# Performance work log

Hardware: AMD Instinct MI355X
Metric: run time of the kernel (lower is better)

## Reference

```python
import jax, jax.numpy as jnp
import numpy as np

B, T, H, DH = 4, 2048, 16, 128
D = H * DH            # inner_dim = 2048
F = 4096              # mlp_inner_dim
E = 8                 # num_expert_mlp
TOP_K = 2


def setup_inputs() -> dict:
    key = jax.random.key(0)
    ks = jax.random.split(key, 5)
    s_in = 1.0 / np.sqrt(D)
    s_f = 1.0 / np.sqrt(F)
    return {
        "stm": jax.random.normal(ks[0], (B, T, H, DH), dtype=jnp.float32),
        "gate_w": jax.random.normal(ks[1], (E, D), dtype=jnp.float32) * s_in,
        "w1": jax.random.normal(ks[2], (E, F, D), dtype=jnp.float32) * s_in,
        "w2": jax.random.normal(ks[3], (E, D, F), dtype=jnp.float32) * s_f,
        "w3": jax.random.normal(ks[4], (E, F, D), dtype=jnp.float32) * s_in,
    }


def reference(stm, gate_w, w1, w2, w3):
    b, t, h, dh = stm.shape
    d = h * dh
    x = stm.reshape(b * t, d)                                   # [N, D]
    logits = x @ gate_w.T                                       # [N, E]
    top_logit, top_idx = jax.lax.top_k(logits, TOP_K)           # [N, 2]
    gw = jax.nn.softmax(top_logit.astype(jnp.float32), axis=1).astype(x.dtype)
    out = jnp.zeros_like(x)
    n_expert = w1.shape[0]
    for e in range(n_expert):
        # combine weight for expert e per token (0 if not routed)
        we = jnp.sum(jnp.where(top_idx == e, gw, jnp.zeros_like(gw)), axis=1)  # [N]
        gate = jax.nn.silu(x @ w1[e].T)                          # [N, F]
        up = x @ w3[e].T                                         # [N, F]
        y = (gate * up) @ w2[e].T                                # [N, D]
        out = out + we[:, None] * y
    return out.reshape(b, t, h, dh)
```

## Files before the change

kernel.cpp:

```cpp
#include <hip/hip_runtime.h>
#include <hip/hip_bf16.h>
#include <stdint.h>

#define N_TOK 8192
#define DIM   2048
#define FDIM  4096
#define NEXP  8

#define XB_OFF   0ull
#define HB_OFF   33554432ull
#define WB1_OFF  176160768ull
#define WB3_OFF  243269632ull
#define META_OFF 310378496ull
#define CNT_OFF   (META_OFF)
#define EBASE_OFF (META_OFF + 64ull)
#define ELIST_OFF (META_OFF + 128ull)
#define EWTS_OFF  (ELIST_OFF + 262144ull)

typedef float f32x4 __attribute__((ext_vector_type(4)));
typedef short s16x8 __attribute__((ext_vector_type(8)));

__device__ __forceinline__ uint32_t pkbf(float a, float b) {
  uint32_t ua = __builtin_bit_cast(uint32_t, a) + 0x8000u;
  uint32_t ub = __builtin_bit_cast(uint32_t, b) + 0x8000u;
  return (ua >> 16) | (ub & 0xffff0000u);
}

__device__ __forceinline__ void gld16(const void* g, void* l) {
  __builtin_amdgcn_global_load_lds(
      (__attribute__((address_space(1))) void*)g,
      (__attribute__((address_space(3))) void*)l, 16, 0, 0);
}

__global__ void zero_out_k(float* out) {
  const size_t i = ((size_t)blockIdx.x * 256 + threadIdx.x) * 4;
  *(float4*)(out + i) = make_float4(0.f, 0.f, 0.f, 0.f);
}

__global__ void init_k(int* cnt) {
  if (threadIdx.x < NEXP) cnt[threadIdx.x] = 0;
}

__global__ void router_k(const float* __restrict__ x, const float* __restrict__ gw,
                         __hip_bfloat16* __restrict__ xb, int* __restrict__ cnt,
                         int* __restrict__ elist, float* __restrict__ ewts) {
  const int n = blockIdx.x;
  const int t = threadIdx.x;
  const float* xr = x + (size_t)n * DIM;
  const float4 v0 = *(const float4*)(xr + t * 8);
  const float4 v1 = *(const float4*)(xr + t * 8 + 4);
  uint4 u;
  u.x = pkbf(v0.x, v0.y); u.y = pkbf(v0.z, v0.w);
  u.z = pkbf(v1.x, v1.y); u.w = pkbf(v1.z, v1.w);
  *(uint4*)(xb + (size_t)n * DIM + t * 8) = u;

  float p[NEXP];
#pragma unroll
  for (int e = 0; e < NEXP; ++e) {
    const float* g = gw + e * DIM + t * 8;
    const float4 g0 = *(const float4*)g;
    const float4 g1 = *(const float4*)(g + 4);
    p[e] = v0.x * g0.x + v0.y * g0.y + v0.z * g0.z + v0.w * g0.w +
           v1.x * g1.x + v1.y * g1.y + v1.z * g1.z + v1.w * g1.w;
  }
#pragma unroll
  for (int off = 32; off >= 1; off >>= 1)
#pragma unroll
    for (int e = 0; e < NEXP; ++e) p[e] += __shfl_xor(p[e], off, 64);

  __shared__ float red[4][NEXP];
  const int lane = t & 63, wv = t >> 6;
  if (lane == 0) {
#pragma unroll
    for (int e = 0; e < NEXP; ++e) red[wv][e] = p[e];
  }
  __syncthreads();
  if (t == 0) {
    float l0 = -1e30f, l1 = -1e30f;
    int e0 = 0, e1 = 0;
#pragma unroll
    for (int e = 0; e < NEXP; ++e) {
      float v = red[0][e] + red[1][e] + red[2][e] + red[3][e];
      if (v > l0) { l1 = l0; e1 = e0; l0 = v; e0 = e; }
      else if (v > l1) { l1 = v; e1 = e; }
    }
    const float ed = expf(l1 - l0);
    const float inv = 1.f / (1.f + ed);
    int s0 = atomicAdd(cnt + e0, 1);
    elist[e0 * N_TOK + s0] = n;
    ewts[e0 * N_TOK + s0] = inv;
    int s1 = atomicAdd(cnt + e1, 1);
    elist[e1 * N_TOK + s1] = (int)((uint32_t)n | 0x80000000u);
    ewts[e1 * N_TOK + s1] = ed * inv;
  }
}

__global__ void scan_k(const int* __restrict__ cnt, int* __restrict__ ebase) {
  if (threadIdx.x == 0 && blockIdx.x == 0) {
    int b = 0;
    for (int e = 0; e < NEXP; ++e) { ebase[e] = b; b += (cnt[e] + 127) & ~127; }
  }
}

__global__ void convW_k(const float* __restrict__ src, __hip_bfloat16* __restrict__ dst,
                        int r0, int nrh, int rtot, int kd) {
  const int cpr = kd / 8;
  const int total = NEXP * nrh * cpr;
  for (int i = blockIdx.x * blockDim.x + threadIdx.x; i < total;
       i += gridDim.x * blockDim.x) {
    const int e = i / (nrh * cpr);
    const int rem = i - e * nrh * cpr;
    const int lr = rem / cpr;
    const int c = rem - lr * cpr;
    const float* s = src + ((size_t)e * rtot + r0 + lr) * (size_t)kd + c * 8;
    const float4 a = *(const float4*)s;
    const float4 b = *(const float4*)(s + 4);
    uint4 u;
    u.x = pkbf(a.x, a.y); u.y = pkbf(a.z, a.w);
    u.z = pkbf(b.x, b.y); u.w = pkbf(b.z, b.w);
    *(uint4*)(dst + ((size_t)e * nrh + lr) * (size_t)kd + c * 8) = u;
  }
}

__global__ __launch_bounds__(256, 2) void moe_up_k(
    const __hip_bfloat16* __restrict__ xb, const __hip_bfloat16* __restrict__ w1b,
    const __hip_bfloat16* __restrict__ w3b, __hip_bfloat16* __restrict__ hb,
    const int* __restrict__ cnt, const int* __restrict__ ebase,
    const int* __restrict__ elist, int noff) {
  constexpr int NT = DIM / 32;
  const int e = blockIdx.z;
  const int count = cnt[e];
  const int mt = blockIdx.y;
  if (mt * 128 >= count) return;
  const int bn0 = blockIdx.x * 128;
  const int ncol0 = noff + bn0;

  __shared__ char lds[73728];
  const int t = threadIdx.x;
  const int lane = t & 63, wv = t >> 6;
  const int wr = wv >> 1, wc = wv & 1;
  const int* lst = elist + e * N_TOK;
  const size_t hrow0 = (size_t)ebase[e] + (size_t)mt * 128;

  const int r0 = t >> 2;
  const int ks = (t & 3) ^ ((r0 >> 1) & 3);
  size_t sA[2], sB1[2];
  int ldsO[2];
#pragma unroll
  for (int i = 0; i < 2; ++i) {
    const int r = r0 + i * 64;
    int idx = mt * 128 + r;
    if (idx >= count) idx = 0;
    const size_t tok = (size_t)(lst[idx] & 0x7fffffff);
    sA[i] = tok * DIM + ks * 8;
    sB1[i] = ((size_t)e * 2048 + bn0 + r) * DIM + ks * 8;
    ldsO[i] = i * 4096 + wv * 1024;
  }

  const int fr = lane & 15;
  const int swzc = ((lane >> 4) ^ ((fr >> 1) & 3)) << 4;
  const int aoff = (wr * 64 + fr) * 64 + swzc;
  const int boff = (wc * 64 + fr) * 64 + swzc;

  f32x4 accG[4][4], accU[4][4];
#pragma unroll
  for (int mi = 0; mi < 4; ++mi)
#pragma unroll
    for (int ni = 0; ni < 4; ++ni) {
      accG[mi][ni] = {0.f, 0.f, 0.f, 0.f};
      accU[mi][ni] = {0.f, 0.f, 0.f, 0.f};
    }

  auto stage = [&](int kt, int b) {
    const int k0 = kt * 32;
    char* base = lds + b * 24576;
#pragma unroll
    for (int i = 0; i < 2; ++i)
      gld16(xb + sA[i] + k0, base + ldsO[i]);
#pragma unroll
    for (int i = 0; i < 2; ++i)
      gld16(w1b + sB1[i] + k0, base + 8192 + ldsO[i]);
#pragma unroll
    for (int i = 0; i < 2; ++i)
      gld16(w3b + sB1[i] + k0, base + 16384 + ldsO[i]);
  };

  stage(0, 0);
  stage(1, 1);
  asm volatile("s_waitcnt vmcnt(6)" ::: "memory");
  __builtin_amdgcn_sched_barrier(0);
  __builtin_amdgcn_s_barrier();
  __builtin_amdgcn_sched_barrier(0);

  int bR = 0, bS = 2;
#pragma unroll 3
  for (int kt = 0; kt < NT; ++kt) {
    const int t2 = (kt + 2 < NT) ? kt + 2 : NT - 1;
    stage(t2, bS);
    char* base = lds + bR * 24576;
    s16x8 af[4], b1f[4], b3f[4];
#pragma unroll
    for (int mi = 0; mi < 4; ++mi)
      af[mi] = *(const s16x8*)(base + aoff + mi * 1024);
#pragma unroll
    for (int ni = 0; ni < 4; ++ni) {
      b1f[ni] = *(const s16x8*)(base + 8192 + boff + ni * 1024);
      b3f[ni] = *(const s16x8*)(base + 16384 + boff + ni * 1024);
    }
#pragma unroll
    for (int mi = 0; mi < 4; ++mi)
#pragma unroll
      for (int ni = 0; ni < 4; ++ni) {
        accG[mi][ni] = __builtin_amdgcn_mfma_f32_16x16x32_bf16(
            af[mi], b1f[ni], accG[mi][ni], 0, 0, 0);
        accU[mi][ni] = __builtin_amdgcn_mfma_f32_16x16x32_bf16(
            af[mi], b3f[ni], accU[mi][ni], 0, 0, 0);
      }
    asm volatile("s_waitcnt vmcnt(6)" ::: "memory");
    __builtin_amdgcn_sched_barrier(0);
    __builtin_amdgcn_s_barrier();
    __builtin_amdgcn_sched_barrier(0);
    bR = (bR == 2) ? 0 : bR + 1;
    bS = (bS == 2) ? 0 : bS + 1;
  }

  const int erow = (lane >> 4) * 4;
  const int ecol = lane & 15;
#pragma unroll
  for (int mi = 0; mi < 4; ++mi)
#pragma unroll
    for (int ni = 0; ni < 4; ++ni) {
      const size_t cb = ncol0 + wc * 64 + ni * 16 + ecol;
#pragma unroll
      for (int j = 0; j < 4; ++j) {
        const size_t r = hrow0 + wr * 64 + mi * 16 + erow + j;
        const float g = accG[mi][ni][j];
        const float uu = accU[mi][ni][j];
        const float h = g / (1.f + __expf(-g)) * uu;
        hb[r * FDIM + cb] = __float2bfloat16(h);
      }
    }
}

__global__ __launch_bounds__(256, 2) void moe_down_k(
    const __hip_bfloat16* __restrict__ hb, const __hip_bfloat16* __restrict__ w2b,
    float* __restrict__ out, const int* __restrict__ cnt,
    const int* __restrict__ ebase, const int* __restrict__ elist,
    const float* __restrict__ ewts) {
  constexpr int NT = FDIM / 32;
  const int e = blockIdx.x;
  const int count = cnt[e];
  const int mt = blockIdx.y;
  if (mt * 128 >= count) return;
  const int bn0 = blockIdx.z * 256;

  __shared__ char lds[73728];
  const int t = threadIdx.x;
  const int lane = t & 63, wv = t >> 6;
  const int wr = wv >> 1, wc = wv & 1;
  const int* lst = elist + e * N_TOK;
  const size_t hrow0 = (size_t)ebase[e] + (size_t)mt * 128;

  const int r0 = t >> 2;
  const int ks = (t & 3) ^ ((r0 >> 1) & 3);
  size_t sA[2], sB[2];
  int ldsO[2];
#pragma unroll
  for (int i = 0; i < 2; ++i) {
    const int r = r0 + i * 64;
    sA[i] = (hrow0 + r) * (size_t)FDIM + ks * 8;
    sB[i] = ((size_t)e * 2048 + bn0 + r) * (size_t)FDIM + ks * 8;
    ldsO[i] = i * 4096 + wv * 1024;
  }
  const size_t sBp = 128 * (size_t)FDIM;

  const int fr = lane & 15;
  const int swzc = ((lane >> 4) ^ ((fr >> 1) & 3)) << 4;
  const int aoff = (wr * 64 + fr) * 64 + swzc;
  const int boff = (wc * 64 + fr) * 64 + swzc;

  f32x4 accP[2][4][4];
#pragma unroll
  for (int p = 0; p < 2; ++p)
#pragma unroll
    for (int mi = 0; mi < 4; ++mi)
#pragma unroll
      for (int ni = 0; ni < 4; ++ni) accP[p][mi][ni] = {0.f, 0.f, 0.f, 0.f};

  auto stage = [&](int kt, int b) {
    const int k0 = kt * 32;
    char* base = lds + b * 24576;
#pragma unroll
    for (int i = 0; i < 2; ++i)
      gld16(hb + sA[i] + k0, base + ldsO[i]);
#pragma unroll
    for (int i = 0; i < 2; ++i)
      gld16(w2b + sB[i] + k0, base + 8192 + ldsO[i]);
#pragma unroll
    for (int i = 0; i < 2; ++i)
      gld16(w2b + sB[i] + sBp + k0, base + 16384 + ldsO[i]);
  };

  stage(0, 0);
  stage(1, 1);
  asm volatile("s_waitcnt vmcnt(6)" ::: "memory");
  __builtin_amdgcn_sched_barrier(0);
  __builtin_amdgcn_s_barrier();
  __builtin_amdgcn_sched_barrier(0);

  int bR = 0, bS = 2;
#pragma unroll 3
  for (int kt = 0; kt < NT; ++kt) {
    const int t2 = (kt + 2 < NT) ? kt + 2 : NT - 1;
    stage(t2, bS);
    char* base = lds + bR * 24576;
    s16x8 af[4], b0f[4], b1f[4];
#pragma unroll
    for (int mi = 0; mi < 4; ++mi)
      af[mi] = *(const s16x8*)(base + aoff + mi * 1024);
#pragma unroll
    for (int ni = 0; ni < 4; ++ni) {
      b0f[ni] = *(const s16x8*)(base + 8192 + boff + ni * 1024);
      b1f[ni] = *(const s16x8*)(base + 16384 + boff + ni * 1024);
    }
#pragma unroll
    for (int mi = 0; mi < 4; ++mi)
#pragma unroll
      for (int ni = 0; ni < 4; ++ni) {
        accP[0][mi][ni] = __builtin_amdgcn_mfma_f32_16x16x32_bf16(
            af[mi], b0f[ni], accP[0][mi][ni], 0, 0, 0);
        accP[1][mi][ni] = __builtin_amdgcn_mfma_f32_16x16x32_bf16(
            af[mi], b1f[ni], accP[1][mi][ni], 0, 0, 0);
      }
    asm volatile("s_waitcnt vmcnt(6)" ::: "memory");
    __builtin_amdgcn_sched_barrier(0);
    __builtin_amdgcn_s_barrier();
    __builtin_amdgcn_sched_barrier(0);
    bR = (bR == 2) ? 0 : bR + 1;
    bS = (bS == 2) ? 0 : bS + 1;
  }

  const int erow = (lane >> 4) * 4;
  const int ecol = lane & 15;
#pragma unroll
  for (int mi = 0; mi < 4; ++mi)
#pragma unroll
    for (int j = 0; j < 4; ++j) {
      const int i = mt * 128 + wr * 64 + mi * 16 + erow + j;
      if (i < count) {
        const uint32_t info = (uint32_t)lst[i];
        const int tok = (int)(info & 0x7fffffffu);
        const float wt = ewts[e * N_TOK + i];
        float* prow = out + (size_t)tok * DIM;
#pragma unroll
        for (int p = 0; p < 2; ++p)
#pragma unroll
          for (int ni = 0; ni < 4; ++ni) {
            const int cb = bn0 + p * 128 + wc * 64 + ni * 16 + ecol;
            atomicAdd(prow + cb, wt * accP[p][mi][ni][j]);
          }
      }
    }
}

extern "C" void kernel_launch(void* const* d_in, const int* in_sizes, int n_in,
                              void* d_out, int out_size, void* d_ws, size_t ws_size,
                              hipStream_t stream) {
  const float* stm = (const float*)d_in[0];
  const float* gw = (const float*)d_in[1];
  const float* w1 = (const float*)d_in[2];
  const float* w2 = (const float*)d_in[3];
  const float* w3 = (const float*)d_in[4];
  float* out = (float*)d_out;
  char* ws = (char*)d_ws;

  __hip_bfloat16* xb = (__hip_bfloat16*)(ws + XB_OFF);
  __hip_bfloat16* hb = (__hip_bfloat16*)(ws + HB_OFF);
  __hip_bfloat16* wb1 = (__hip_bfloat16*)(ws + WB1_OFF);
  __hip_bfloat16* wb3 = (__hip_bfloat16*)(ws + WB3_OFF);
  __hip_bfloat16* w2full = (__hip_bfloat16*)(ws + WB1_OFF);
  int* cnt = (int*)(ws + CNT_OFF);
  int* ebase = (int*)(ws + EBASE_OFF);
  int* elist = (int*)(ws + ELIST_OFF);
  float* ewts = (float*)(ws + EWTS_OFF);

  init_k<<<1, 64, 0, stream>>>(cnt);
  router_k<<<N_TOK, 256, 0, stream>>>(stm, gw, xb, cnt, elist, ewts);
  scan_k<<<1, 64, 0, stream>>>(cnt, ebase);
  zero_out_k<<<N_TOK * DIM / 1024, 256, 0, stream>>>(out);

  const dim3 gUp(16, 64, 8);
  const dim3 gDn(8, 64, 8);

  convW_k<<<2048, 256, 0, stream>>>(w1, wb1, 0, 2048, FDIM, DIM);
  convW_k<<<2048, 256, 0, stream>>>(w3, wb3, 0, 2048, FDIM, DIM);
  moe_up_k<<<gUp, 256, 0, stream>>>(xb, wb1, wb3, hb, cnt, ebase, elist, 0);
  convW_k<<<2048, 256, 0, stream>>>(w1, wb1, 2048, 2048, FDIM, DIM);
  convW_k<<<2048, 256, 0, stream>>>(w3, wb3, 2048, 2048, FDIM, DIM);
  moe_up_k<<<gUp, 256, 0, stream>>>(xb, wb1, wb3, hb, cnt, ebase, elist, 2048);

  convW_k<<<4096, 256, 0, stream>>>(w2, w2full, 0, 2048, DIM, FDIM);
  moe_down_k<<<gDn, 256, 0, stream>>>(hb, w2full, out, cnt, ebase, elist, ewts);
}
```

Before: 1.349 ms.

## Overlap fp32-to-bf16 weight conversion with GEMM kernels via double-buffered quarters

Removes the standalone weight-conversion and zeroing kernels. The conversion of the next weight quarter (or half) now runs inside extra blocks of the preceding router, up-projection or down-projection launch, using two ping-pong workspace buffers. Output zeroing is folded into the router launch as well. The aim is to hide conversion bandwidth behind GEMM compute and cut serial kernel launches. The cost is smaller GEMM launches (four up and two down) with more tail effects, and converter blocks competing with GEMM blocks for the same CUs.

```diff
diff --git a/kernel.cpp b/kernel.cpp
--- a/kernel.cpp
+++ b/kernel.cpp
@@ -9,14 +9,16 @@
 
 #define XB_OFF   0ull
 #define HB_OFF   33554432ull
-#define WB1_OFF  176160768ull
-#define WB3_OFF  243269632ull
+#define WQ0_OFF  176160768ull
+#define WQ1_OFF  243269632ull
 #define META_OFF 310378496ull
 #define CNT_OFF   (META_OFF)
 #define EBASE_OFF (META_OFF + 64ull)
 #define ELIST_OFF (META_OFF + 128ull)
 #define EWTS_OFF  (ELIST_OFF + 262144ull)
 
+#define W3Q_ELEMS 16777216
+
 typedef float f32x4 __attribute__((ext_vector_type(4)));
 typedef short s16x8 __attribute__((ext_vector_type(8)));
 
@@ -32,82 +34,11 @@
       (__attribute__((address_space(3))) void*)l, 16, 0, 0);
 }
 
-__global__ void zero_out_k(float* out) {
-  const size_t i = ((size_t)blockIdx.x * 256 + threadIdx.x) * 4;
-  *(float4*)(out + i) = make_float4(0.f, 0.f, 0.f, 0.f);
-}
-
-__global__ void init_k(int* cnt) {
-  if (threadIdx.x < NEXP) cnt[threadIdx.x] = 0;
-}
-
-__global__ void router_k(const float* __restrict__ x, const float* __restrict__ gw,
-                         __hip_bfloat16* __restrict__ xb, int* __restrict__ cnt,
-                         int* __restrict__ elist, float* __restrict__ ewts) {
-  const int n = blockIdx.x;
-  const int t = threadIdx.x;
-  const float* xr = x + (size_t)n * DIM;
-  const float4 v0 = *(const float4*)(xr + t * 8);
-  const float4 v1 = *(const float4*)(xr + t * 8 + 4);
-  uint4 u;
-  u.x = pkbf(v0.x, v0.y); u.y = pkbf(v0.z, v0.w);
-  u.z = pkbf(v1.x, v1.y); u.w = pkbf(v1.z, v1.w);
-  *(uint4*)(xb + (size_t)n * DIM + t * 8) = u;
-
-  float p[NEXP];
-#pragma unroll
-  for (int e = 0; e < NEXP; ++e) {
-    const float* g = gw + e * DIM + t * 8;
-    const float4 g0 = *(const float4*)g;
-    const float4 g1 = *(const float4*)(g + 4);
-    p[e] = v0.x * g0.x + v0.y * g0.y + v0.z * g0.z + v0.w * g0.w +
-           v1.x * g1.x + v1.y * g1.y + v1.z * g1.z + v1.w * g1.w;
-  }
-#pragma unroll
-  for (int off = 32; off >= 1; off >>= 1)
-#pragma unroll
-    for (int e = 0; e < NEXP; ++e) p[e] += __shfl_xor(p[e], off, 64);
-
-  __shared__ float red[4][NEXP];
-  const int lane = t & 63, wv = t >> 6;
-  if (lane == 0) {
-#pragma unroll
-    for (int e = 0; e < NEXP; ++e) red[wv][e] = p[e];
-  }
-  __syncthreads();
-  if (t == 0) {
-    float l0 = -1e30f, l1 = -1e30f;
-    int e0 = 0, e1 = 0;
-#pragma unroll
-    for (int e = 0; e < NEXP; ++e) {
-      float v = red[0][e] + red[1][e] + red[2][e] + red[3][e];
-      if (v > l0) { l1 = l0; e1 = e0; l0 = v; e0 = e; }
-      else if (v > l1) { l1 = v; e1 = e; }
-    }
-    const float ed = expf(l1 - l0);
-    const float inv = 1.f / (1.f + ed);
-    int s0 = atomicAdd(cnt + e0, 1);
-    elist[e0 * N_TOK + s0] = n;
-    ewts[e0 * N_TOK + s0] = inv;
-    int s1 = atomicAdd(cnt + e1, 1);
-    elist[e1 * N_TOK + s1] = (int)((uint32_t)n | 0x80000000u);
-    ewts[e1 * N_TOK + s1] = ed * inv;
-  }
-}
-
-__global__ void scan_k(const int* __restrict__ cnt, int* __restrict__ ebase) {
-  if (threadIdx.x == 0 && blockIdx.x == 0) {
-    int b = 0;
-    for (int e = 0; e < NEXP; ++e) { ebase[e] = b; b += (cnt[e] + 127) & ~127; }
-  }
-}
-
-__global__ void convW_k(const float* __restrict__ src, __hip_bfloat16* __restrict__ dst,
-                        int r0, int nrh, int rtot, int kd) {
+__device__ __forceinline__ void conv_chunks(
+    const float* __restrict__ src, __hip_bfloat16* __restrict__ dst,
+    int r0, int nrh, int rtot, int kd, int idx0, int stride, int total) {
   const int cpr = kd / 8;
-  const int total = NEXP * nrh * cpr;
-  for (int i = blockIdx.x * blockDim.x + threadIdx.x; i < total;
-       i += gridDim.x * blockDim.x) {
+  for (int i = idx0; i < total; i += stride) {
     const int e = i / (nrh * cpr);
     const int rem = i - e * nrh * cpr;
     const int lr = rem / cpr;
@@ -122,18 +53,112 @@
   }
 }
 
+__global__ void init_k(int* cnt) {
+  if (threadIdx.x < NEXP) cnt[threadIdx.x] = 0;
+}
+
+__global__ void router_k(const float* __restrict__ x, const float* __restrict__ gw,
+                         __hip_bfloat16* __restrict__ xb, int* __restrict__ cnt,
+                         int* __restrict__ elist, float* __restrict__ ewts,
+                         const float* __restrict__ w1, const float* __restrict__ w3,
+                         __hip_bfloat16* __restrict__ wq0, float* __restrict__ out) {
+  const int blk = blockIdx.x;
+  const int t = threadIdx.x;
+  if (blk >= N_TOK) {
+    const int cb = blk - N_TOK;
+    if (cb < 2048) {
+      conv_chunks(w1, wq0, 0, 1024, FDIM, DIM, cb * 256 + t, 2048 * 256, 2097152);
+    } else if (cb < 4096) {
+      conv_chunks(w3, wq0 + W3Q_ELEMS, 0, 1024, FDIM, DIM,
+                  (cb - 2048) * 256 + t, 2048 * 256, 2097152);
+    } else {
+      for (size_t i = (size_t)(cb - 4096) * 256 + t; i < 4194304; i += 512 * 256)
+        *(float4*)(out + i * 4) = make_float4(0.f, 0.f, 0.f, 0.f);
+    }
+    return;
+  }
+  const int n = blk;
+  const float* xr = x + (size_t)n * DIM;
+  const float4 v0 = *(const float4*)(xr + t * 8);
+  const float4 v1 = *(const float4*)(xr + t * 8 + 4);
+  uint4 u;
+  u.x = pkbf(v0.x, v0.y); u.y = pkbf(v0.z, v0.w);
+  u.z = pkbf(v1.x, v1.y); u.w = pkbf(v1.z, v1.w);
+  *(uint4*)(xb + (size_t)n * DIM + t * 8) = u;
+
+  float p[NEXP];
+#pragma unroll
+  for (int e = 0; e < NEXP; ++e) {
+    const float* g = gw + e * DIM + t * 8;
+    const float4 g0 = *(const float4*)g;
+    const float4 g1 = *(const float4*)(g + 4);
+    p[e] = v0.x * g0.x + v0.y * g0.y + v0.z * g0.z + v0.w * g0.w +
+           v1.x * g1.x + v1.y * g1.y + v1.z * g1.z + v1.w * g1.w;
+  }
+#pragma unroll
+  for (int off = 32; off >= 1; off >>= 1)
+#pragma unroll
+    for (int e = 0; e < NEXP; ++e) p[e] += __shfl_xor(p[e], off, 64);
+
+  __shared__ float red[4][NEXP];
+  const int lane = t & 63, wv = t >> 6;
+  if (lane == 0) {
+#pragma unroll
+    for (int e = 0; e < NEXP; ++e) red[wv][e] = p[e];
+  }
+  __syncthreads();
+  if (t == 0) {
+    float l0 = -1e30f, l1 = -1e30f;
+    int e0 = 0, e1 = 0;
+#pragma unroll
+    for (int e = 0; e < NEXP; ++e) {
+      float v = red[0][e] + red[1][e] + red[2][e] + red[3][e];
+      if (v > l0) { l1 = l0; e1 = e0; l0 = v; e0 = e; }
+      else if (v > l1) { l1 = v; e1 = e; }
+    }
+    const float ed = expf(l1 - l0);
+    const float inv = 1.f / (1.f + ed);
+    int s0 = atomicAdd(cnt + e0, 1);
+    elist[e0 * N_TOK + s0] = n;
+    ewts[e0 * N_TOK + s0] = inv;
+    int s1 = atomicAdd(cnt + e1, 1);
+    elist[e1 * N_TOK + s1] = (int)((uint32_t)n | 0x80000000u);
+    ewts[e1 * N_TOK + s1] = ed * inv;
+  }
+}
+
+__global__ void scan_k(const int* __restrict__ cnt, int* __restrict__ ebase) {
+  if (threadIdx.x == 0 && blockIdx.x == 0) {
+    int b = 0;
+    for (int e = 0; e < NEXP; ++e) { ebase[e] = b; b += (cnt[e] + 127) & ~127; }
+  }
+}
+
 __global__ __launch_bounds__(256, 2) void moe_up_k(
-    const __hip_bfloat16* __restrict__ xb, const __hip_bfloat16* __restrict__ w1b,
-    const __hip_bfloat16* __restrict__ w3b, __hip_bfloat16* __restrict__ hb,
-    const int* __restrict__ cnt, const int* __restrict__ ebase,
-    const int* __restrict__ elist, int noff) {
+    const __hip_bfloat16* __restrict__ xb, const __hip_bfloat16* __restrict__ wq,
+    __hip_bfloat16* __restrict__ wnext, const float* __restrict__ w1,
+    const float* __restrict__ w3, const float* __restrict__ w2,
+    __hip_bfloat16* __restrict__ hb, const int* __restrict__ cnt,
+    const int* __restrict__ ebase, const int* __restrict__ elist, int qn) {
   constexpr int NT = DIM / 32;
+  if (blockIdx.x >= 8) {
+    const int cb = (blockIdx.x - 8) + 8 * (blockIdx.y + 64 * blockIdx.z);
+    const int idx0 = cb * 256 + threadIdx.x;
+    if (qn < 3) {
+      const int r0 = (qn + 1) * 1024;
+      conv_chunks(w1, wnext, r0, 1024, FDIM, DIM, idx0, 4096 * 256, 2097152);
+      conv_chunks(w3, wnext + W3Q_ELEMS, r0, 1024, FDIM, DIM, idx0, 4096 * 256, 2097152);
+    } else {
+      conv_chunks(w2, wnext, 0, 1024, DIM, FDIM, idx0, 4096 * 256, 4194304);
+    }
+    return;
+  }
   const int e = blockIdx.z;
   const int count = cnt[e];
   const int mt = blockIdx.y;
   if (mt * 128 >= count) return;
   const int bn0 = blockIdx.x * 128;
-  const int ncol0 = noff + bn0;
+  const int ncol0 = qn * 1024 + bn0;
 
   __shared__ char lds[73728];
   const int t = threadIdx.x;
@@ -153,7 +178,7 @@
     if (idx >= count) idx = 0;
     const size_t tok = (size_t)(lst[idx] & 0x7fffffff);
     sA[i] = tok * DIM + ks * 8;
-    sB1[i] = ((size_t)e * 2048 + bn0 + r) * DIM + ks * 8;
+    sB1[i] = ((size_t)e * 1024 + bn0 + r) * DIM + ks * 8;
     ldsO[i] = i * 4096 + wv * 1024;
   }
 
@@ -179,10 +204,10 @@
       gld16(xb + sA[i] + k0, base + ldsO[i]);
 #pragma unroll
     for (int i = 0; i < 2; ++i)
-      gld16(w1b + sB1[i] + k0, base + 8192 + ldsO[i]);
-#pragma unroll
-    for (int i = 0; i < 2; ++i)
-      gld16(w3b + sB1[i] + k0, base + 16384 + ldsO[i]);
+      gld16(wq + sB1[i] + k0, base + 8192 + ldsO[i]);
+#pragma unroll
+    for (int i = 0; i < 2; ++i)
+      gld16(wq + W3Q_ELEMS + sB1[i] + k0, base + 16384 + ldsO[i]);
   };
 
   stage(0, 0);
@@ -243,11 +268,18 @@
 }
 
 __global__ __launch_bounds__(256, 2) void moe_down_k(
-    const __hip_bfloat16* __restrict__ hb, const __hip_bfloat16* __restrict__ w2b,
+    const __hip_bfloat16* __restrict__ hb, const __hip_bfloat16* __restrict__ w2h,
+    __hip_bfloat16* __restrict__ wnext, const float* __restrict__ w2,
     float* __restrict__ out, const int* __restrict__ cnt,
     const int* __restrict__ ebase, const int* __restrict__ elist,
-    const float* __restrict__ ewts) {
+    const float* __restrict__ ewts, int half) {
   constexpr int NT = FDIM / 32;
+  if (blockIdx.z >= 4) {
+    const int cb = blockIdx.x + 8 * (blockIdx.y + 64 * (blockIdx.z - 4));
+    conv_chunks(w2, wnext, 1024, 1024, DIM, FDIM,
+                cb * 256 + threadIdx.x, 2048 * 256, 4194304);
+    return;
+  }
   const int e = blockIdx.x;
   const int count = cnt[e];
   const int mt = blockIdx.y;
@@ -269,7 +301,7 @@
   for (int i = 0; i < 2; ++i) {
     const int r = r0 + i * 64;
     sA[i] = (hrow0 + r) * (size_t)FDIM + ks * 8;
-    sB[i] = ((size_t)e * 2048 + bn0 + r) * (size_t)FDIM + ks * 8;
+    sB[i] = ((size_t)e * 1024 + bn0 + r) * (size_t)FDIM + ks * 8;
     ldsO[i] = i * 4096 + wv * 1024;
   }
   const size_t sBp = 128 * (size_t)FDIM;
@@ -295,10 +327,10 @@
       gld16(hb + sA[i] + k0, base + ldsO[i]);
 #pragma unroll
     for (int i = 0; i < 2; ++i)
-      gld16(w2b + sB[i] + k0, base + 8192 + ldsO[i]);
-#pragma unroll
-    for (int i = 0; i < 2; ++i)
-      gld16(w2b + sB[i] + sBp + k0, base + 16384 + ldsO[i]);
+      gld16(w2h + sB[i] + k0, base + 8192 + ldsO[i]);
+#pragma unroll
+    for (int i = 0; i < 2; ++i)
+      gld16(w2h + sB[i] + sBp + k0, base + 16384 + ldsO[i]);
   };
 
   stage(0, 0);
@@ -356,7 +388,7 @@
         for (int p = 0; p < 2; ++p)
 #pragma unroll
           for (int ni = 0; ni < 4; ++ni) {
-            const int cb = bn0 + p * 128 + wc * 64 + ni * 16 + ecol;
+            const int cb = half * 1024 + bn0 + p * 128 + wc * 64 + ni * 16 + ecol;
             atomicAdd(prow + cb, wt * accP[p][mi][ni][j]);
           }
       }
@@ -376,29 +408,27 @@
 
   __hip_bfloat16* xb = (__hip_bfloat16*)(ws + XB_OFF);
   __hip_bfloat16* hb = (__hip_bfloat16*)(ws + HB_OFF);
-  __hip_bfloat16* wb1 = (__hip_bfloat16*)(ws + WB1_OFF);
-  __hip_bfloat16* wb3 = (__hip_bfloat16*)(ws + WB3_OFF);
-  __hip_bfloat16* w2full = (__hip_bfloat16*)(ws + WB1_OFF);
+  __hip_bfloat16* wq[2] = {(__hip_bfloat16*)(ws + WQ0_OFF),
+                           (__hip_bfloat16*)(ws + WQ1_OFF)};
   int* cnt = (int*)(ws + CNT_OFF);
   int* ebase = (int*)(ws + EBASE_OFF);
   int* elist = (int*)(ws + ELIST_OFF);
   float* ewts = (float*)(ws + EWTS_OFF);
 
   init_k<<<1, 64, 0, stream>>>(cnt);
-  router_k<<<N_TOK, 256, 0, stream>>>(stm, gw, xb, cnt, elist, ewts);
+  router_k<<<N_TOK + 4608, 256, 0, stream>>>(stm, gw, xb, cnt, elist, ewts,
+                                             w1, w3, wq[0], out);
   scan_k<<<1, 64, 0, stream>>>(cnt, ebase);
-  zero_out_k<<<N_TOK * DIM / 1024, 256, 0, stream>>>(out);
 
   const dim3 gUp(16, 64, 8);
-  const dim3 gDn(8, 64, 8);
-
-  convW_k<<<2048, 256, 0, stream>>>(w1, wb1, 0, 2048, FDIM, DIM);
-  convW_k<<<2048, 256, 0, stream>>>(w3, wb3, 0, 2048, FDIM, DIM);
-  moe_up_k<<<gUp, 256, 0, stream>>>(xb, wb1, wb3, hb, cnt, ebase, elist, 0);
-  convW_k<<<2048, 256, 0, stream>>>(w1, wb1, 2048, 2048, FDIM, DIM);
-  convW_k<<<2048, 256, 0, stream>>>(w3, wb3, 2048, 2048, FDIM, DIM);
-  moe_up_k<<<gUp, 256, 0, stream>>>(xb, wb1, wb3, hb, cnt, ebase, elist, 2048);
-
-  convW_k<<<4096, 256, 0, stream>>>(w2, w2full, 0, 2048, DIM, FDIM);
-  moe_down_k<<<gDn, 256, 0, stream>>>(hb, w2full, out, cnt, ebase, elist, ewts);
-}
+  for (int q = 0; q < 4; ++q)
+    moe_up_k<<<gUp, 256, 0, stream>>>(xb, wq[q & 1], wq[(q + 1) & 1],
+                                      w1, w3, w2, hb, cnt, ebase, elist, q);
+
+  const dim3 gDn0(8, 64, 8);
+  const dim3 gDn1(8, 64, 4);
+  moe_down_k<<<gDn0, 256, 0, stream>>>(hb, wq[0], wq[1], w2, out,
+                                       cnt, ebase, elist, ewts, 0);
+  moe_down_k<<<gDn1, 256, 0, stream>>>(hb, wq[1], wq[1], w2, out,
+                                       cnt, ebase, elist, ewts, 1);
+}
```

New measurement: 1.819 ms. 34.8% more time.

## Fuse weight conversion and output zeroing into router, split down-proj by F halves

Applied to the files above, without the earlier changes.

The first-half w1/w3 bf16 conversion and the output zeroing now run as extra blocks of the router kernel, so they overlap with routing instead of running as separate launches. The w1+w3 conversions for the second half are merged into one kernel. The down projection is split into two K-halves over F, each using a half-size converted slice of w2, with the workspace buffers rotated between halves. This removes launches and tail bubbles and keeps the workspace small, at the cost of two partial down-projection passes that both accumulate into the output.

```diff
diff --git a/kernel.cpp b/kernel.cpp
--- a/kernel.cpp
+++ b/kernel.cpp
@@ -9,8 +9,8 @@
 
 #define XB_OFF   0ull
 #define HB_OFF   33554432ull
-#define WB1_OFF  176160768ull
-#define WB3_OFF  243269632ull
+#define WQA_OFF  176160768ull
+#define WQB_OFF  243269632ull
 #define META_OFF 310378496ull
 #define CNT_OFF   (META_OFF)
 #define EBASE_OFF (META_OFF + 64ull)
@@ -32,82 +32,11 @@
       (__attribute__((address_space(3))) void*)l, 16, 0, 0);
 }
 
-__global__ void zero_out_k(float* out) {
-  const size_t i = ((size_t)blockIdx.x * 256 + threadIdx.x) * 4;
-  *(float4*)(out + i) = make_float4(0.f, 0.f, 0.f, 0.f);
-}
-
-__global__ void init_k(int* cnt) {
-  if (threadIdx.x < NEXP) cnt[threadIdx.x] = 0;
-}
-
-__global__ void router_k(const float* __restrict__ x, const float* __restrict__ gw,
-                         __hip_bfloat16* __restrict__ xb, int* __restrict__ cnt,
-                         int* __restrict__ elist, float* __restrict__ ewts) {
-  const int n = blockIdx.x;
-  const int t = threadIdx.x;
-  const float* xr = x + (size_t)n * DIM;
-  const float4 v0 = *(const float4*)(xr + t * 8);
-  const float4 v1 = *(const float4*)(xr + t * 8 + 4);
-  uint4 u;
-  u.x = pkbf(v0.x, v0.y); u.y = pkbf(v0.z, v0.w);
-  u.z = pkbf(v1.x, v1.y); u.w = pkbf(v1.z, v1.w);
-  *(uint4*)(xb + (size_t)n * DIM + t * 8) = u;
-
-  float p[NEXP];
-#pragma unroll
-  for (int e = 0; e < NEXP; ++e) {
-    const float* g = gw + e * DIM + t * 8;
-    const float4 g0 = *(const float4*)g;
-    const float4 g1 = *(const float4*)(g + 4);
-    p[e] = v0.x * g0.x + v0.y * g0.y + v0.z * g0.z + v0.w * g0.w +
-           v1.x * g1.x + v1.y * g1.y + v1.z * g1.z + v1.w * g1.w;
-  }
-#pragma unroll
-  for (int off = 32; off >= 1; off >>= 1)
-#pragma unroll
-    for (int e = 0; e < NEXP; ++e) p[e] += __shfl_xor(p[e], off, 64);
-
-  __shared__ float red[4][NEXP];
-  const int lane = t & 63, wv = t >> 6;
-  if (lane == 0) {
-#pragma unroll
-    for (int e = 0; e < NEXP; ++e) red[wv][e] = p[e];
-  }
-  __syncthreads();
-  if (t == 0) {
-    float l0 = -1e30f, l1 = -1e30f;
-    int e0 = 0, e1 = 0;
-#pragma unroll
-    for (int e = 0; e < NEXP; ++e) {
-      float v = red[0][e] + red[1][e] + red[2][e] + red[3][e];
-      if (v > l0) { l1 = l0; e1 = e0; l0 = v; e0 = e; }
-      else if (v > l1) { l1 = v; e1 = e; }
-    }
-    const float ed = expf(l1 - l0);
-    const float inv = 1.f / (1.f + ed);
-    int s0 = atomicAdd(cnt + e0, 1);
-    elist[e0 * N_TOK + s0] = n;
-    ewts[e0 * N_TOK + s0] = inv;
-    int s1 = atomicAdd(cnt + e1, 1);
-    elist[e1 * N_TOK + s1] = (int)((uint32_t)n | 0x80000000u);
-    ewts[e1 * N_TOK + s1] = ed * inv;
-  }
-}
-
-__global__ void scan_k(const int* __restrict__ cnt, int* __restrict__ ebase) {
-  if (threadIdx.x == 0 && blockIdx.x == 0) {
-    int b = 0;
-    for (int e = 0; e < NEXP; ++e) { ebase[e] = b; b += (cnt[e] + 127) & ~127; }
-  }
-}
-
-__global__ void convW_k(const float* __restrict__ src, __hip_bfloat16* __restrict__ dst,
-                        int r0, int nrh, int rtot, int kd) {
+__device__ __forceinline__ void conv_chunks(
+    const float* __restrict__ src, __hip_bfloat16* __restrict__ dst,
+    int r0, int nrh, int rtot, int kd, int idx0, int stride, int total) {
   const int cpr = kd / 8;
-  const int total = NEXP * nrh * cpr;
-  for (int i = blockIdx.x * blockDim.x + threadIdx.x; i < total;
-       i += gridDim.x * blockDim.x) {
+  for (int i = idx0; i < total; i += stride) {
     const int e = i / (nrh * cpr);
     const int rem = i - e * nrh * cpr;
     const int lr = rem / cpr;
@@ -119,6 +48,114 @@
     u.x = pkbf(a.x, a.y); u.y = pkbf(a.z, a.w);
     u.z = pkbf(b.x, b.y); u.w = pkbf(b.z, b.w);
     *(uint4*)(dst + ((size_t)e * nrh + lr) * (size_t)kd + c * 8) = u;
+  }
+}
+
+__global__ void init_k(int* cnt) {
+  if (threadIdx.x < NEXP) cnt[threadIdx.x] = 0;
+}
+
+__global__ void convH_k(const float* __restrict__ w1, __hip_bfloat16* __restrict__ d1,
+                        const float* __restrict__ w3, __hip_bfloat16* __restrict__ d3,
+                        int r0) {
+  const int idx0 = blockIdx.x * 256 + threadIdx.x;
+  conv_chunks(w1, d1, r0, 2048, FDIM, DIM, idx0, 4096 * 256, 4194304);
+  conv_chunks(w3, d3, r0, 2048, FDIM, DIM, idx0, 4096 * 256, 4194304);
+}
+
+__global__ void convW2_k(const float* __restrict__ w2, __hip_bfloat16* __restrict__ dst,
+                         int col0) {
+  const int total = NEXP * DIM * 256;
+  for (int i = blockIdx.x * blockDim.x + threadIdx.x; i < total;
+       i += gridDim.x * blockDim.x) {
+    const int e = i / (DIM * 256);
+    const int rem = i - e * DIM * 256;
+    const int lr = rem >> 8;
+    const int c = rem & 255;
+    const float* s = w2 + ((size_t)e * DIM + lr) * (size_t)FDIM + col0 + c * 8;
+    const float4 a = *(const float4*)s;
+    const float4 b = *(const float4*)(s + 4);
+    uint4 u;
+    u.x = pkbf(a.x, a.y); u.y = pkbf(a.z, a.w);
+    u.z = pkbf(b.x, b.y); u.w = pkbf(b.z, b.w);
+    *(uint4*)(dst + ((size_t)e * DIM + lr) * 2048 + c * 8) = u;
+  }
+}
+
+__global__ void router_k(const float* __restrict__ x, const float* __restrict__ gw,
+                         __hip_bfloat16* __restrict__ xb, int* __restrict__ cnt,
+                         int* __restrict__ elist, float* __restrict__ ewts,
+                         const float* __restrict__ w1, const float* __restrict__ w3,
+                         __hip_bfloat16* __restrict__ wA, __hip_bfloat16* __restrict__ wB,
+                         float* __restrict__ out) {
+  const int blk = blockIdx.x;
+  const int t = threadIdx.x;
+  if (blk >= N_TOK) {
+    const int cb = blk - N_TOK;
+    if (cb < 4096) {
+      conv_chunks(w1, wA, 0, 2048, FDIM, DIM, cb * 256 + t, 4096 * 256, 4194304);
+    } else if (cb < 8192) {
+      conv_chunks(w3, wB, 0, 2048, FDIM, DIM, (cb - 4096) * 256 + t, 4096 * 256, 4194304);
+    } else {
+      for (size_t i = (size_t)(cb - 8192) * 256 + t; i < 4194304; i += 512 * 256)
+        *(float4*)(out + i * 4) = make_float4(0.f, 0.f, 0.f, 0.f);
+    }
+    return;
+  }
+  const int n = blk;
+  const float* xr = x + (size_t)n * DIM;
+  const float4 v0 = *(const float4*)(xr + t * 8);
+  const float4 v1 = *(const float4*)(xr + t * 8 + 4);
+  uint4 u;
+  u.x = pkbf(v0.x, v0.y); u.y = pkbf(v0.z, v0.w);
+  u.z = pkbf(v1.x, v1.y); u.w = pkbf(v1.z, v1.w);
+  *(uint4*)(xb + (size_t)n * DIM + t * 8) = u;
+
+  float p[NEXP];
+#pragma unroll
+  for (int e = 0; e < NEXP; ++e) {
+    const float* g = gw + e * DIM + t * 8;
+    const float4 g0 = *(const float4*)g;
+    const float4 g1 = *(const float4*)(g + 4);
+    p[e] = v0.x * g0.x + v0.y * g0.y + v0.z * g0.z + v0.w * g0.w +
+           v1.x * g1.x + v1.y * g1.y + v1.z * g1.z + v1.w * g1.w;
+  }
+#pragma unroll
+  for (int off = 32; off >= 1; off >>= 1)
+#pragma unroll
+    for (int e = 0; e < NEXP; ++e) p[e] += __shfl_xor(p[e], off, 64);
+
+  __shared__ float red[4][NEXP];
+  const int lane = t & 63, wv = t >> 6;
+  if (lane == 0) {
+#pragma unroll
+    for (int e = 0; e < NEXP; ++e) red[wv][e] = p[e];
+  }
+  __syncthreads();
+  if (t == 0) {
+    float l0 = -1e30f, l1 = -1e30f;
+    int e0 = 0, e1 = 0;
+#pragma unroll
+    for (int e = 0; e < NEXP; ++e) {
+      float v = red[0][e] + red[1][e] + red[2][e] + red[3][e];
+      if (v > l0) { l1 = l0; e1 = e0; l0 = v; e0 = e; }
+      else if (v > l1) { l1 = v; e1 = e; }
+    }
+    const float ed = expf(l1 - l0);
+    const float inv = 1.f / (1.f + ed);
+    int s0 = atomicAdd(cnt + e0, 1);
+    elist[e0 * N_TOK + s0] = n;
+    ewts[e0 * N_TOK + s0] = inv;
+    int s1 = atomicAdd(cnt + e1, 1);
+    elist[e1 * N_TOK + s1] = (int)((uint32_t)n | 0x80000000u);
+    ewts[e1 * N_TOK + s1] = ed * inv;
+  }
+}
+
+__global__ void scan_k(const int* __restrict__ cnt, int* __restrict__ ebase) {
+  if (threadIdx.x == 0 && blockIdx.x == 0) {
+    int b = 0;
+    for (int e = 0; e < NEXP; ++e) { ebase[e] = b; b += (cnt[e] + 127) & ~127; }
   }
 }
 
@@ -243,11 +280,11 @@
 }
 
 __global__ __launch_bounds__(256, 2) void moe_down_k(
-    const __hip_bfloat16* __restrict__ hb, const __hip_bfloat16* __restrict__ w2b,
+    const __hip_bfloat16* __restrict__ hb, const __hip_bfloat16* __restrict__ w2h,
     float* __restrict__ out, const int* __restrict__ cnt,
     const int* __restrict__ ebase, const int* __restrict__ elist,
-    const float* __restrict__ ewts) {
-  constexpr int NT = FDIM / 32;
+    const float* __restrict__ ewts, int half) {
+  constexpr int NT = 2048 / 32;
   const int e = blockIdx.x;
   const int count = cnt[e];
   const int mt = blockIdx.y;
@@ -268,11 +305,11 @@
 #pragma unroll
   for (int i = 0; i < 2; ++i) {
     const int r = r0 + i * 64;
-    sA[i] = (hrow0 + r) * (size_t)FDIM + ks * 8;
-    sB[i] = ((size_t)e * 2048 + bn0 + r) * (size_t)FDIM + ks * 8;
+    sA[i] = (hrow0 + r) * (size_t)FDIM + half * 2048 + ks * 8;
+    sB[i] = ((size_t)e * DIM + bn0 + r) * 2048 + ks * 8;
     ldsO[i] = i * 4096 + wv * 1024;
   }
-  const size_t sBp = 128 * (size_t)FDIM;
+  const size_t sBp = 128 * 2048;
 
   const int fr = lane & 15;
   const int swzc = ((lane >> 4) ^ ((fr >> 1) & 3)) << 4;
@@ -295,10 +332,10 @@
       gld16(hb + sA[i] + k0, base + ldsO[i]);
 #pragma unroll
     for (int i = 0; i < 2; ++i)
-      gld16(w2b + sB[i] + k0, base + 8192 + ldsO[i]);
-#pragma unroll
-    for (int i = 0; i < 2; ++i)
-      gld16(w2b + sB[i] + sBp + k0, base + 16384 + ldsO[i]);
+      gld16(w2h + sB[i] + k0, base + 8192 + ldsO[i]);
+#pragma unroll
+    for (int i = 0; i < 2; ++i)
+      gld16(w2h + sB[i] + sBp + k0, base + 16384 + ldsO[i]);
   };
 
   stage(0, 0);
@@ -376,29 +413,29 @@
 
   __hip_bfloat16* xb = (__hip_bfloat16*)(ws + XB_OFF);
   __hip_bfloat16* hb = (__hip_bfloat16*)(ws + HB_OFF);
-  __hip_bfloat16* wb1 = (__hip_bfloat16*)(ws + WB1_OFF);
-  __hip_bfloat16* wb3 = (__hip_bfloat16*)(ws + WB3_OFF);
-  __hip_bfloat16* w2full = (__hip_bfloat16*)(ws + WB1_OFF);
+  __hip_bfloat16* wA = (__hip_bfloat16*)(ws + WQA_OFF);
+  __hip_bfloat16* wB = (__hip_bfloat16*)(ws + WQB_OFF);
   int* cnt = (int*)(ws + CNT_OFF);
   int* ebase = (int*)(ws + EBASE_OFF);
   int* elist = (int*)(ws + ELIST_OFF);
   float* ewts = (float*)(ws + EWTS_OFF);
 
   init_k<<<1, 64, 0, stream>>>(cnt);
-  router_k<<<N_TOK, 256, 0, stream>>>(stm, gw, xb, cnt, elist, ewts);
+  router_k<<<N_TOK + 8704, 256, 0, stream>>>(stm, gw, xb, cnt, elist, ewts,
+                                             w1, w3, wA, wB, out);
   scan_k<<<1, 64, 0, stream>>>(cnt, ebase);
-  zero_out_k<<<N_TOK * DIM / 1024, 256, 0, stream>>>(out);
 
   const dim3 gUp(16, 64, 8);
   const dim3 gDn(8, 64, 8);
 
-  convW_k<<<2048, 256, 0, stream>>>(w1, wb1, 0, 2048, FDIM, DIM);
-  convW_k<<<2048, 256, 0, stream>>>(w3, wb3, 0, 2048, FDIM, DIM);
-  moe_up_k<<<gUp, 256, 0, stream>>>(xb, wb1, wb3, hb, cnt, ebase, elist, 0);
-  convW_k<<<2048, 256, 0, stream>>>(w1, wb1, 2048, 2048, FDIM, DIM);
-  convW_k<<<2048, 256, 0, stream>>>(w3, wb3, 2048, 2048, FDIM, DIM);
-  moe_up_k<<<gUp, 256, 0, stream>>>(xb, wb1, wb3, hb, cnt, ebase, elist, 2048);
-
-  convW_k<<<4096, 256, 0, stream>>>(w2, w2full, 0, 2048, DIM, FDIM);
-  moe_down_k<<<gDn, 256, 0, stream>>>(hb, w2full, out, cnt, ebase, elist, ewts);
-}
+  moe_up_k<<<gUp, 256, 0, stream>>>(xb, wA, wB, hb, cnt, ebase, elist, 0);
+
+  convW2_k<<<2048, 256, 0, stream>>>(w2, wA, 0);
+  moe_down_k<<<gDn, 256, 0, stream>>>(hb, wA, out, cnt, ebase, elist, ewts, 0);
+
+  convH_k<<<4096, 256, 0, stream>>>(w1, wB, w3, wA, 2048);
+  moe_up_k<<<gUp, 256, 0, stream>>>(xb, wB, wA, hb, cnt, ebase, elist, 2048);
+
+  convW2_k<<<2048, 256, 0, stream>>>(w2, wB, 2048);
+  moe_down_k<<<gDn, 256, 0, stream>>>(hb, wB, out, cnt, ebase, elist, ewts, 1);
+}
```

Result: slower. 1.417 ms (+5.0%).
